# Performance work log

Hardware: AMD Instinct MI355X
Metric: run time of the kernel (lower is better)

## Reference

```python
import jax, jax.numpy as jnp
import numpy as np

B, N, F, H, R = 16, 64, 64, 4, 50
C = F * H  # n_coefficients = n_heads * hidden_features
CUTOFF = 5.0  # ExpNormalSmearing cutoff_upper (cutoff_lower = 0)


def _dense(k, fin, fout):
    s = 1.0 / np.sqrt(fin)
    return jax.random.uniform(k, (fin, fout), jnp.float32, -s, s)


def setup_inputs() -> dict:
    key = jax.random.key(0)
    ks = jax.random.split(key, 20)
    start = float(np.exp(-CUTOFF))
    return {
        "h": jax.random.normal(ks[0], (B, N, F), jnp.float32),
        "x": jax.random.normal(ks[1], (B, N, 3), jnp.float32),
        "v": jax.random.normal(ks[2], (B, N, 3), jnp.float32) * 0.1,
        # edge model (ContinuousFilterConvolutionWithConcatenation)
        "W_in": _dense(ks[3], 2 * F, R), "b_in": jnp.zeros((R,), jnp.float32),
        "rbf_means": jnp.linspace(start, 1.0, R).astype(jnp.float32),
        "rbf_betas": jnp.full((R,), (2.0 / R * (1.0 - start)) ** -2, jnp.float32),
        "W_e1": _dense(ks[4], 2 * F + R + 1, F), "b_e1": jnp.zeros((F,), jnp.float32),
        "W_e2": _dense(ks[5], F, F), "b_e2": jnp.zeros((F,), jnp.float32),
        # semantic attention
        "W_sem": _dense(ks[6], F, H), "b_sem": jnp.zeros((H,), jnp.float32),
        "log_gamma": -jnp.log(jnp.linspace(1.0, 5.0, H)).astype(jnp.float32),
        # spatial attention
        "W_xmix": _dense(ks[7], C, C),
        "W_post1": _dense(ks[8], C, F), "b_post1": jnp.zeros((F,), jnp.float32),
        "W_post2": _dense(ks[9], F, F), "b_post2": jnp.zeros((F,), jnp.float32),
        # node update
        "W_node1": _dense(ks[10], F + C + F, F), "b_node1": jnp.zeros((F,), jnp.float32),
        "W_node2": _dense(ks[11], F, F), "b_node2": jnp.zeros((F,), jnp.float32),
        # velocity update
        "W_vel1": _dense(ks[12], F, F), "b_vel1": jnp.zeros((F,), jnp.float32),
        "W_vel2": _dense(ks[13], F, 1),
        "W_vmix": _dense(ks[14], C, 1),
    }


def reference(h, x, v, W_in, b_in, rbf_means, rbf_betas, W_e1, b_e1, W_e2, b_e2,
              W_sem, b_sem, log_gamma, W_xmix, W_post1, b_post1, W_post2, b_post2,
              W_node1, b_node1, W_node2, b_node2, W_vel1, b_vel1, W_vel2, W_vmix):
    silu = jax.nn.silu
    n = h.shape[-2]
    # pairwise displacement x_j - x_i : (B, N, N, 3)
    x_minus_xt = x[..., None, :, :] - x[..., :, None, :]
    d = jnp.sqrt(jax.nn.relu((x_minus_xt ** 2).sum(-1, keepdims=True)) + 1e-5)  # (B,N,N,1)
    # pairwise node features [h_j, h_i] : (B, N, N, 2F)
    hj = jnp.broadcast_to(h[..., None, :, :], h.shape[:-2] + (n, n, h.shape[-1]))
    hi = jnp.broadcast_to(h[..., :, None, :], hj.shape)
    h_cat = jnp.concatenate([hj, hi], -1)
    # edge model: RBF-smeared continuous-filter conv with concatenation
    h_mid = h_cat @ W_in + b_in  # (B,N,N,R)
    cut = 0.5 * (jnp.cos(d * (jnp.pi / CUTOFF)) + 1.0) * (d < CUTOFF)
    rbf = cut * jnp.exp(-rbf_betas * (jnp.exp(-d) - rbf_means) ** 2)  # (B,N,N,R)
    h_e = jnp.concatenate([h_cat, rbf * h_mid, d], -1)
    h_e = silu(h_e @ W_e1 + b_e1) @ W_e2 + b_e2  # (B,N,N,F)
    # attentions, softmax over neighbor axis (-2), diagonal masked out
    eye = jnp.eye(n, dtype=h.dtype)[:, :, None]
    sem = jax.nn.celu(h_e @ W_sem + b_sem, alpha=2.0) - 1e5 * eye
    sem = jax.nn.softmax(sem, axis=-2)  # (B,N,N,H)
    euc = jax.nn.softmax(-(d + 1e5 * eye) * jnp.exp(log_gamma), axis=-2)  # (B,N,N,H)
    att = euc * sem
    att = att / att.sum(-2, keepdims=True)
    # per-head attention-weighted edge features, flattened (F outer, H inner)
    h_e_att = (h_e[..., :, None] * att[..., None, :]).reshape(att.shape[:-1] + (F * H,))
    # spatial attention on unit displacement vectors
    coeff = jnp.tanh(h_e_att @ W_xmix)  # (B,N,N,C)
    x_hat = x_minus_xt / (d + 1e-5)
    comb = x_hat[..., None, :] * coeff[..., None]  # (B,N,N,C,3)
    comb_sum = comb.mean(axis=-3)  # mean over neighbors -> (B,N,C,3)
    h_comb = (comb_sum ** 2).sum(-1)  # invariant squared norms (B,N,C)
    h_comb = silu(silu(h_comb @ W_post1 + b_post1) @ W_post2 + b_post2)
    # node update (residual)
    h_agg = h_e_att.sum(axis=-2)  # (B,N,C)
    h_out = h + silu(silu(jnp.concatenate([h, h_agg, h_comb], -1) @ W_node1 + b_node1) @ W_node2 + b_node2)
    # equivariant velocity / coordinate update
    delta_v = jnp.einsum('...ijcd,c->...id', comb, W_vmix[:, 0]) / n  # v_mixing + mean over j
    gate = 2.0 * jax.nn.sigmoid(silu(h_out @ W_vel1 + b_vel1) @ W_vel2)  # double_sigmoid, (B,N,1)
    v_out = delta_v + gate * v
    x_out = x + v_out
    return h_out, x_out, v_out
```

## Files before the change

### kernel.cpp

```cpp
#include <hip/hip_runtime.h>
#include <math.h>

#define NB 16
#define NN 64
#define NF 64
#define NH 4
#define NR 50
#define NC 256

typedef __attribute__((ext_vector_type(8))) short short8;
typedef __attribute__((ext_vector_type(4))) float f32x4;

#define WS_WE1R 0
#define WS_WE2  4096
#define WS_WX   8192
#define WS_PO1  73728
#define WS_NO1  90112
#define WS_PO2  114688
#define WS_NO2  118784
#define WS_VE1  122880
#define MID_F   65536
#define E1_F    (MID_F + 131072)
#define HAGG_F  (E1_F + 131072)
#define COMB_F  (HAGG_F + 262144)

__device__ __forceinline__ float siluf(float x) { return x / (1.f + __expf(-x)); }
__device__ __forceinline__ float tanhfast(float x) { return 1.f - 2.f / (__expf(2.f * x) + 1.f); }

__device__ __forceinline__ short f2bfs(float f) {
    __bf16 b = (__bf16)f;
    union { __bf16 b; short s; } u; u.b = b; return u.s;
}
__device__ __forceinline__ float bf1(ushort u) {
    union { unsigned u; float f; } c; c.u = ((unsigned)u) << 16; return c.f;
}
__device__ __forceinline__ float bflo(unsigned u) {
    union { unsigned u; float f; } c; c.u = u << 16; return c.f;
}
__device__ __forceinline__ float bfhi(unsigned u) {
    union { unsigned u; float f; } c; c.u = u & 0xFFFF0000u; return c.f;
}

__device__ __forceinline__ float wave_max(float v) {
#pragma unroll
    for (int s = 32; s >= 1; s >>= 1) v = fmaxf(v, __shfl_xor(v, s));
    return v;
}
__device__ __forceinline__ float wave_sum(float v) {
#pragma unroll
    for (int s = 32; s >= 1; s >>= 1) v += __shfl_xor(v, s);
    return v;
}

__global__ __launch_bounds__(256)
void prep_kernel(const float* __restrict__ W_e1, const float* __restrict__ b_e1,
                 const float* __restrict__ W_e2, const float* __restrict__ W_xmix,
                 const float* __restrict__ W_post1, const float* __restrict__ W_node1,
                 const float* __restrict__ W_post2, const float* __restrict__ W_node2,
                 const float* __restrict__ W_vel1,
                 const float* __restrict__ h, const float* __restrict__ W_in,
                 const float* __restrict__ b_in,
                 short* __restrict__ wpack, float* __restrict__ mid_T, float* __restrict__ e1)
{
    int blk = blockIdx.x, t = threadIdx.x;
    if (blk < 62) {
        int s = blk * 256 + t;
        short8 val;
        if (s < 512) {
            int cl = s & 15, g = (s >> 4) & 3, q = s >> 6;
            int ks = q & 1, nt = q >> 1;
            int c = nt * 16 + cl, k0 = 32 * ks + 8 * g;
#pragma unroll
            for (int i = 0; i < 8; i++) {
                int kr = k0 + i;
                float f = (kr < 50) ? W_e1[(128 + kr) * NF + c] : (kr == 50 ? W_e1[178 * NF + c] : 0.f);
                val[i] = f2bfs(f);
            }
            *(short8*)(&wpack[WS_WE1R + s * 8]) = val;
        } else if (s < 1024) {
            int u = s - 512;
            int cl = u & 15, g = (u >> 4) & 3, q = u >> 6;
            int ks = q & 1, nt = q >> 1;
            int c = nt * 16 + cl, k0 = 32 * ks + 8 * g;
#pragma unroll
            for (int i = 0; i < 8; i++) val[i] = f2bfs(W_e2[(k0 + i) * NF + c]);
            *(short8*)(&wpack[WS_WE2 + u * 8]) = val;
        } else if (s < 9216) {
            int u = s - 1024;
            int cl = u & 15, g = (u >> 4) & 3, q = u >> 6;
            int ks = q & 7, wn = q >> 3;
            int c = (wn >> 2) * 64 + (wn & 3) * 16 + cl, k0 = 32 * ks + 8 * g;
#pragma unroll
            for (int i = 0; i < 8; i++) val[i] = f2bfs(W_xmix[(k0 + i) * NC + c]);
            *(short8*)(&wpack[WS_WX + u * 8]) = val;
        } else if (s < 11264) {
            int u = s - 9216;
            int cl = u & 15, g = (u >> 4) & 3, q = u >> 6;
            int ks = q & 7, nt = q >> 3;
            int c = nt * 16 + cl, k0 = 32 * ks + 8 * g;
#pragma unroll
            for (int i = 0; i < 8; i++) val[i] = f2bfs(W_post1[(k0 + i) * NF + c]);
            *(short8*)(&wpack[WS_PO1 + u * 8]) = val;
        } else if (s < 14336) {
            int u = s - 11264;
            int cl = u & 15, g = (u >> 4) & 3, q = u >> 6;
            int ks = q % 12, nt = q / 12;
            int c = nt * 16 + cl, k0 = 32 * ks + 8 * g;
#pragma unroll
            for (int i = 0; i < 8; i++) val[i] = f2bfs(W_node1[(k0 + i) * NF + c]);
            *(short8*)(&wpack[WS_NO1 + u * 8]) = val;
        } else if (s < 14848) {
            int u = s - 14336;
            int cl = u & 15, g = (u >> 4) & 3, q = u >> 6;
            int ks = q & 1, nt = q >> 1;
            int c = nt * 16 + cl, k0 = 32 * ks + 8 * g;
#pragma unroll
            for (int i = 0; i < 8; i++) val[i] = f2bfs(W_post2[(k0 + i) * NF + c]);
            *(short8*)(&wpack[WS_PO2 + u * 8]) = val;
        } else if (s < 15360) {
            int u = s - 14848;
            int cl = u & 15, g = (u >> 4) & 3, q = u >> 6;
            int ks = q & 1, nt = q >> 1;
            int c = nt * 16 + cl, k0 = 32 * ks + 8 * g;
#pragma unroll
            for (int i = 0; i < 8; i++) val[i] = f2bfs(W_node2[(k0 + i) * NF + c]);
            *(short8*)(&wpack[WS_NO2 + u * 8]) = val;
        } else {
            int u = s - 15360;
            int cl = u & 15, g = (u >> 4) & 3, q = u >> 6;
            int ks = q & 1, nt = q >> 1;
            int c = nt * 16 + cl, k0 = 32 * ks + 8 * g;
#pragma unroll
            for (int i = 0; i < 8; i++) val[i] = f2bfs(W_vel1[(k0 + i) * NF + c]);
            *(short8*)(&wpack[WS_VE1 + u * 8]) = val;
        }
    } else {
        int node = blk - 62;
        __shared__ float s_hn[64];
        if (t < 64) s_hn[t] = h[node * NF + t];
        __syncthreads();
        if (t < 64) {
            float acc = 0.f;
#pragma unroll 8
            for (int k = 0; k < 64; k++) acc += s_hn[k] * W_e1[k * NF + t];
            e1[node * 128 + t] = acc;
        } else if (t < 128) {
            int f = t - 64;
            float acc = b_e1[f];
#pragma unroll 8
            for (int k = 0; k < 64; k++) acc += s_hn[k] * W_e1[(64 + k) * NF + f];
            e1[node * 128 + 64 + f] = acc;
        } else if (t < 178) {
            int r = t - 128;
            float acc = 0.f;
#pragma unroll 8
            for (int k = 0; k < 64; k++) acc += s_hn[k] * W_in[k * NR + r];
            mid_T[r * 1024 + node] = acc;
        } else if (t >= 192 && t < 242) {
            int r = t - 192;
            float acc = b_in[r];
#pragma unroll 8
            for (int k = 0; k < 64; k++) acc += s_hn[k] * W_in[(64 + k) * NR + r];
            mid_T[(64 + r) * 1024 + node] = acc;
        }
    }
}

__global__ __launch_bounds__(256)
void sake_edge_kernel(
    const float* __restrict__ x,
    const float* __restrict__ mid_T, const float* __restrict__ e1,
    const float* __restrict__ rbf_means, const float* __restrict__ rbf_betas,
    const float* __restrict__ b_e2,
    const float* __restrict__ W_sem, const float* __restrict__ b_sem,
    const float* __restrict__ log_gamma,
    const short* __restrict__ wpack,
    float* __restrict__ hagg_g, float* __restrict__ comb_g)
{
    const int bi = blockIdx.x;
    const int b  = bi >> 6;
    const int i  = bi & 63;
    const int t  = threadIdx.x;
    const int w  = t >> 6, l = t & 63, lr = l & 15, lg = l >> 4;

    __shared__ __align__(16) short s_A[16 * 64 * 8];
    __shared__ __align__(16) short s_he[64 * 72];
    __shared__ float s_xhat[256];
    __shared__ float s_att[256];
    __shared__ float s_wsem[256];
    __shared__ float s_midi[52];

    const short8* A8  = (const short8*)s_A;
    short8*       A8w = (short8*)s_A;
    const short8* We1p = (const short8*)(wpack + WS_WE1R);
    const short8* We2p = (const short8*)(wpack + WS_WE2);
    const short8* Wxp  = (const short8*)(wpack + WS_WX);

    s_wsem[t] = W_sem[t];
    if (t < 50) s_midi[t] = mid_T[(64 + t) * 1024 + b * 64 + i];
    if (t < 64) {
        int j = t;
        float dx = x[(b * NN + j) * 3 + 0] - x[(b * NN + i) * 3 + 0];
        float dy = x[(b * NN + j) * 3 + 1] - x[(b * NN + i) * 3 + 1];
        float dz = x[(b * NN + j) * 3 + 2] - x[(b * NN + i) * 3 + 2];
        float d2 = dx * dx + dy * dy + dz * dz;
        float d  = sqrtf(fmaxf(d2, 0.f) + 1e-5f);
        float inv = 1.f / (d + 1e-5f);
        s_xhat[j * 4 + 0] = dx * inv;
        s_xhat[j * 4 + 1] = dy * inv;
        s_xhat[j * 4 + 2] = dz * inv;
        s_xhat[j * 4 + 3] = d;
    }
    __syncthreads();

    {
        int j = t & 63, p = t >> 6;
        float d = s_xhat[j * 4 + 3];
        float cut = 0.5f * (__cosf(d * 0.6283185307179586f) + 1.f) * (d < 5.f ? 1.f : 0.f);
        float emd = __expf(-d);
        const float* mcol = mid_T + b * 64 + j;
#pragma unroll
        for (int q = 0; q < 2; q++) {
            int sl = 2 * p + q;
            short8 val;
#pragma unroll
            for (int e = 0; e < 8; e++) {
                int r = sl * 8 + e;
                float o;
                if (r < 50) {
                    float m = mcol[r * 1024] + s_midi[r];
                    float df = emd - rbf_means[r];
                    o = cut * __expf(-rbf_betas[r] * df * df) * m;
                } else if (r == 50) o = d;
                else o = 0.f;
                val[e] = f2bfs(o);
            }
            A8w[sl * 64 + j] = val;
        }
    }
    __syncthreads();

    {
        int f = w * 16 + lr;
        const float* e1b = e1 + (size_t)b * 64 * 128;
        float e1i_v = e1b[i * 128 + 64 + f];
        f32x4 acc[4];
#pragma unroll
        for (int jt = 0; jt < 4; jt++)
#pragma unroll
            for (int r = 0; r < 4; r++) {
                int j = jt * 16 + lg * 4 + r;
                acc[jt][r] = e1b[j * 128 + f] + e1i_v;
            }
#pragma unroll
        for (int ks = 0; ks < 2; ks++) {
            short8 bb = We1p[(w * 2 + ks) * 64 + l];
#pragma unroll
            for (int jt = 0; jt < 4; jt++) {
                short8 aa = A8[(ks * 4 + lg) * 64 + jt * 16 + lr];
                acc[jt] = __builtin_amdgcn_mfma_f32_16x16x32_bf16(aa, bb, acc[jt], 0, 0, 0);
            }
        }
#pragma unroll
        for (int jt = 0; jt < 4; jt++)
#pragma unroll
            for (int r = 0; r < 4; r++) {
                int j = jt * 16 + lg * 4 + r;
                s_A[(((f >> 3) + 8) * 64 + j) * 8 + (f & 7)] = f2bfs(siluf(acc[jt][r]));
            }
        __syncthreads();
    }

    {
        f32x4 acc[4];
#pragma unroll
        for (int jt = 0; jt < 4; jt++) { acc[jt][0] = 0.f; acc[jt][1] = 0.f; acc[jt][2] = 0.f; acc[jt][3] = 0.f; }
#pragma unroll
        for (int ks = 0; ks < 2; ks++) {
            short8 bb = We2p[(w * 2 + ks) * 64 + l];
#pragma unroll
            for (int jt = 0; jt < 4; jt++) {
                short8 aa = A8[((8 + ks * 4 + lg)) * 64 + jt * 16 + lr];
                acc[jt] = __builtin_amdgcn_mfma_f32_16x16x32_bf16(aa, bb, acc[jt], 0, 0, 0);
            }
        }
        float be2 = b_e2[w * 16 + lr];
        int f = w * 16 + lr;
#pragma unroll
        for (int jt = 0; jt < 4; jt++)
#pragma unroll
            for (int r = 0; r < 4; r++) {
                int j = jt * 16 + lg * 4 + r;
                s_he[j * 72 + f] = f2bfs(acc[jt][r] + be2);
            }
        __syncthreads();
    }

    {
        int hh = w, j = l;
        const short8* hrow = (const short8*)(s_he + j * 72);
        float acc = b_sem[hh];
#pragma unroll
        for (int q = 0; q < 8; q++) {
            short8 hv = hrow[q];
#pragma unroll
            for (int e = 0; e < 8; e++)
                acc += bf1((ushort)hv[e]) * s_wsem[(q * 8 + e) * 4 + hh];
        }
        float cel = fmaxf(acc, 0.f) + fminf(0.f, 2.f * (__expf(0.5f * acc) - 1.f));
        float diag = (j == i) ? 1e5f : 0.f;
        float slog = cel - diag;
        float m1 = wave_max(slog);
        float e1v = __expf(slog - m1);
        float sem = e1v / wave_sum(e1v);
        float gam = __expf(log_gamma[hh]);
        float elog = -(s_xhat[j * 4 + 3] + diag) * gam;
        float m2 = wave_max(elog);
        float e2 = __expf(elog - m2);
        float euc = e2 / wave_sum(e2);
        float a = sem * euc;
        a = a / wave_sum(a);
        s_att[j * 4 + hh] = a;
    }
    __syncthreads();

    {
        int f2 = t >> 3, hh = (t >> 1) & 3, jh = t & 1;
        float a0 = 0.f, a1 = 0.f;
#pragma unroll 8
        for (int jj = 0; jj < 32; jj++) {
            int j = jh * 32 + jj;
            float at = s_att[j * 4 + hh];
            unsigned u = *(const unsigned*)(s_he + j * 72 + 2 * f2);
            a0 += bflo(u) * at;
            a1 += bfhi(u) * at;
        }
        a0 += __shfl_xor(a0, 1);
        a1 += __shfl_xor(a1, 1);
        if (!jh) {
            hagg_g[bi * 256 + (2 * f2) * 4 + hh]     = a0;
            hagg_g[bi * 256 + (2 * f2 + 1) * 4 + hh] = a1;
        }
    }

    f32x4 acc[4][4];
#pragma unroll
    for (int jt = 0; jt < 4; jt++)
#pragma unroll
        for (int nt = 0; nt < 4; nt++) { acc[jt][nt][0] = 0.f; acc[jt][nt][1] = 0.f; acc[jt][nt][2] = 0.f; acc[jt][nt][3] = 0.f; }

    for (int half = 0; half < 2; half++) {
        {
            int j = t & 63, kc = t >> 6;
            float a0 = s_att[j * 4 + 0], a1 = s_att[j * 4 + 1];
            float a2 = s_att[j * 4 + 2], a3 = s_att[j * 4 + 3];
            short8 hv = *(const short8*)(s_he + j * 72 + (half * 32 + kc * 8));
#pragma unroll
            for (int s = 0; s < 4; s++) {
                int sl = kc * 4 + s;
                float h0 = bf1((ushort)hv[2 * s]), h1 = bf1((ushort)hv[2 * s + 1]);
                short8 val;
                val[0] = f2bfs(h0 * a0); val[1] = f2bfs(h0 * a1);
                val[2] = f2bfs(h0 * a2); val[3] = f2bfs(h0 * a3);
                val[4] = f2bfs(h1 * a0); val[5] = f2bfs(h1 * a1);
                val[6] = f2bfs(h1 * a2); val[7] = f2bfs(h1 * a3);
                A8w[sl * 64 + j] = val;
            }
        }
        __syncthreads();
#pragma unroll
        for (int ks = 0; ks < 4; ks++) {
            short8 aa[4], bb[4];
#pragma unroll
            for (int jt = 0; jt < 4; jt++) aa[jt] = A8[(ks * 4 + lg) * 64 + jt * 16 + lr];
#pragma unroll
            for (int nt = 0; nt < 4; nt++) bb[nt] = Wxp[((w * 4 + nt) * 8 + half * 4 + ks) * 64 + l];
#pragma unroll
            for (int jt = 0; jt < 4; jt++)
#pragma unroll
                for (int nt = 0; nt < 4; nt++)
                    acc[jt][nt] = __builtin_amdgcn_mfma_f32_16x16x32_bf16(aa[jt], bb[nt], acc[jt][nt], 0, 0, 0);
        }
        __syncthreads();
    }

    {
#pragma unroll
        for (int nt = 0; nt < 4; nt++) {
            float p0 = 0.f, p1 = 0.f, p2 = 0.f;
#pragma unroll
            for (int jt = 0; jt < 4; jt++)
#pragma unroll
                for (int r = 0; r < 4; r++) {
                    int j = jt * 16 + lg * 4 + r;
                    float th = tanhfast(acc[jt][nt][r]);
                    p0 += s_xhat[j * 4 + 0] * th;
                    p1 += s_xhat[j * 4 + 1] * th;
                    p2 += s_xhat[j * 4 + 2] * th;
                }
            p0 += __shfl_xor(p0, 16); p0 += __shfl_xor(p0, 32);
            p1 += __shfl_xor(p1, 16); p1 += __shfl_xor(p1, 32);
            p2 += __shfl_xor(p2, 16); p2 += __shfl_xor(p2, 32);
            if (lg == 0) {
                int c = w * 64 + nt * 16 + lr;
                float* cg = comb_g + bi * 768 + c * 3;
                cg[0] = p0 * (1.f / 64.f);
                cg[1] = p1 * (1.f / 64.f);
                cg[2] = p2 * (1.f / 64.f);
            }
        }
    }
}

__global__ __launch_bounds__(256)
void sake_tail_kernel(
    const float* __restrict__ h, const float* __restrict__ x, const float* __restrict__ v,
    const float* __restrict__ hagg_g, const float* __restrict__ comb_g,
    const float* __restrict__ b_post1, const float* __restrict__ b_post2,
    const float* __restrict__ b_node1, const float* __restrict__ b_node2,
    const float* __restrict__ b_vel1,
    const float* __restrict__ W_vel2, const float* __restrict__ W_vmix,
    const short* __restrict__ wpack,
    float* __restrict__ out_h, float* __restrict__ out_x, float* __restrict__ out_v)
{
    const int g0 = blockIdx.x * 16;
    const int t = threadIdx.x;
    const int w = t >> 6, l = t & 63, lr = l & 15, lg = l >> 4;

    __shared__ __align__(16) short s_Aa[88 * 16 * 8];
    __shared__ float s_wv[256];
    __shared__ float s_wv2[64];
    __shared__ float s_red[4][16];

    const short8* A8  = (const short8*)s_Aa;
    const short8* PO1p = (const short8*)(wpack + WS_PO1);
    const short8* NO1p = (const short8*)(wpack + WS_NO1);
    const short8* PO2p = (const short8*)(wpack + WS_PO2);
    const short8* NO2p = (const short8*)(wpack + WS_NO2);
    const short8* VE1p = (const short8*)(wpack + WS_VE1);

    {
        s_wv[t] = W_vmix[t];
        if (t < 64) s_wv2[t] = W_vel2[t];
        int n = t & 15, c0 = (t >> 4) * 16;
        const float* cg = comb_g + (g0 + n) * 768;
        const float* ha = hagg_g + (g0 + n) * 256;
#pragma unroll
        for (int cc = 0; cc < 16; cc++) {
            int c = c0 + cc;
            float v0 = cg[c * 3 + 0], v1 = cg[c * 3 + 1], v2 = cg[c * 3 + 2];
            float hcp = v0 * v0 + v1 * v1 + v2 * v2;
            s_Aa[((c >> 3) * 16 + n) * 8 + (c & 7)] = f2bfs(hcp);
            s_Aa[((40 + (c >> 3)) * 16 + n) * 8 + (c & 7)] = f2bfs(ha[c]);
        }
        int f0 = (t >> 4) * 4;
#pragma unroll
        for (int ff = 0; ff < 4; ff++) {
            int f = f0 + ff;
            s_Aa[((32 + (f >> 3)) * 16 + n) * 8 + (f & 7)] = f2bfs(h[(g0 + n) * 64 + f]);
        }
    }
    __syncthreads();

    {
        f32x4 acc = {0.f, 0.f, 0.f, 0.f};
#pragma unroll
        for (int ks = 0; ks < 8; ks++) {
            short8 aa = A8[(ks * 4 + lg) * 16 + lr];
            short8 bb = PO1p[((w * 8 + ks) * 4 + lg) * 16 + lr];
            acc = __builtin_amdgcn_mfma_f32_16x16x32_bf16(aa, bb, acc, 0, 0, 0);
        }
        int f = w * 16 + lr;
        float bp = b_post1[f];
        __syncthreads();
#pragma unroll
        for (int r = 0; r < 4; r++) {
            int n = lg * 4 + r;
            s_Aa[((80 + (f >> 3)) * 16 + n) * 8 + (f & 7)] = f2bfs(siluf(acc[r] + bp));
        }
        __syncthreads();
    }

    {
        f32x4 acc = {0.f, 0.f, 0.f, 0.f};
#pragma unroll
        for (int ks = 0; ks < 2; ks++) {
            short8 aa = A8[((80 + ks * 4 + lg)) * 16 + lr];
            short8 bb = PO2p[((w * 2 + ks) * 4 + lg) * 16 + lr];
            acc = __builtin_amdgcn_mfma_f32_16x16x32_bf16(aa, bb, acc, 0, 0, 0);
        }
        int f = w * 16 + lr;
        float bp = b_post2[f];
#pragma unroll
        for (int r = 0; r < 4; r++) {
            int n = lg * 4 + r;
            s_Aa[((72 + (f >> 3)) * 16 + n) * 8 + (f & 7)] = f2bfs(siluf(acc[r] + bp));
        }
        __syncthreads();
    }

    {
        f32x4 acc = {0.f, 0.f, 0.f, 0.f};
#pragma unroll
        for (int ks = 0; ks < 12; ks++) {
            short8 aa = A8[((32 + ks * 4 + lg)) * 16 + lr];
            short8 bb = NO1p[((w * 12 + ks) * 4 + lg) * 16 + lr];
            acc = __builtin_amdgcn_mfma_f32_16x16x32_bf16(aa, bb, acc, 0, 0, 0);
        }
        int f = w * 16 + lr;
        float bp = b_node1[f];
#pragma unroll
        for (int r = 0; r < 4; r++) {
            int n = lg * 4 + r;
            s_Aa[((f >> 3) * 16 + n) * 8 + (f & 7)] = f2bfs(siluf(acc[r] + bp));
        }
        __syncthreads();
    }

    {
        f32x4 acc = {0.f, 0.f, 0.f, 0.f};
#pragma unroll
        for (int ks = 0; ks < 2; ks++) {
            short8 aa = A8[(ks * 4 + lg) * 16 + lr];
            short8 bb = NO2p[((w * 2 + ks) * 4 + lg) * 16 + lr];
            acc = __builtin_amdgcn_mfma_f32_16x16x32_bf16(aa, bb, acc, 0, 0, 0);
        }
        int f = w * 16 + lr;
        float bp = b_node2[f];
#pragma unroll
        for (int r = 0; r < 4; r++) {
            int n = lg * 4 + r;
            float ho = h[(g0 + n) * 64 + f] + siluf(acc[r] + bp);
            out_h[(g0 + n) * 64 + f] = ho;
            s_Aa[((8 + (f >> 3)) * 16 + n) * 8 + (f & 7)] = f2bfs(ho);
        }
        __syncthreads();
    }

    {
        f32x4 acc = {0.f, 0.f, 0.f, 0.f};
#pragma unroll
        for (int ks = 0; ks < 2; ks++) {
            short8 aa = A8[((8 + ks * 4 + lg)) * 16 + lr];
            short8 bb = VE1p[((w * 2 + ks) * 4 + lg) * 16 + lr];
            acc = __builtin_amdgcn_mfma_f32_16x16x32_bf16(aa, bb, acc, 0, 0, 0);
        }
        int f = w * 16 + lr;
        float bp = b_vel1[f];
        float wv2 = s_wv2[f];
#pragma unroll
        for (int r = 0; r < 4; r++) {
            float p = siluf(acc[r] + bp) * wv2;
            p += __shfl_xor(p, 1); p += __shfl_xor(p, 2);
            p += __shfl_xor(p, 4); p += __shfl_xor(p, 8);
            if (lr == 0) s_red[w][lg * 4 + r] = p;
        }
        __syncthreads();
    }

    {
        int n = t >> 4, q = t & 15;
        float p0 = 0.f, p1 = 0.f, p2 = 0.f;
        const float* cg = comb_g + (g0 + n) * 768;
#pragma unroll
        for (int cc = 0; cc < 16; cc++) {
            int c = q * 16 + cc;
            float wv = s_wv[c];
            p0 += cg[c * 3 + 0] * wv;
            p1 += cg[c * 3 + 1] * wv;
            p2 += cg[c * 3 + 2] * wv;
        }
        p0 += __shfl_xor(p0, 1); p0 += __shfl_xor(p0, 2); p0 += __shfl_xor(p0, 4); p0 += __shfl_xor(p0, 8);
        p1 += __shfl_xor(p1, 1); p1 += __shfl_xor(p1, 2); p1 += __shfl_xor(p1, 4); p1 += __shfl_xor(p1, 8);
        p2 += __shfl_xor(p2, 1); p2 += __shfl_xor(p2, 2); p2 += __shfl_xor(p2, 4); p2 += __shfl_xor(p2, 8);
        if (q == 0) {
            float g = s_red[0][n] + s_red[1][n] + s_red[2][n] + s_red[3][n];
            g = 2.f / (1.f + __expf(-g));
            float dv0 = p0 + g * v[(g0 + n) * 3 + 0];
            float dv1 = p1 + g * v[(g0 + n) * 3 + 1];
            float dv2 = p2 + g * v[(g0 + n) * 3 + 2];
            out_v[(g0 + n) * 3 + 0] = dv0;
            out_v[(g0 + n) * 3 + 1] = dv1;
            out_v[(g0 + n) * 3 + 2] = dv2;
            out_x[(g0 + n) * 3 + 0] = x[(g0 + n) * 3 + 0] + dv0;
            out_x[(g0 + n) * 3 + 1] = x[(g0 + n) * 3 + 1] + dv1;
            out_x[(g0 + n) * 3 + 2] = x[(g0 + n) * 3 + 2] + dv2;
        }
    }
}

extern "C" void kernel_launch(void* const* d_in, const int* in_sizes, int n_in,
                              void* d_out, int out_size, void* d_ws, size_t ws_size,
                              hipStream_t stream) {
    const float* h        = (const float*)d_in[0];
    const float* x        = (const float*)d_in[1];
    const float* v        = (const float*)d_in[2];
    const float* W_in     = (const float*)d_in[3];
    const float* b_in     = (const float*)d_in[4];
    const float* rbf_m    = (const float*)d_in[5];
    const float* rbf_b    = (const float*)d_in[6];
    const float* W_e1     = (const float*)d_in[7];
    const float* b_e1     = (const float*)d_in[8];
    const float* W_e2     = (const float*)d_in[9];
    const float* b_e2     = (const float*)d_in[10];
    const float* W_sem    = (const float*)d_in[11];
    const float* b_sem    = (const float*)d_in[12];
    const float* log_g    = (const float*)d_in[13];
    const float* W_xmix   = (const float*)d_in[14];
    const float* W_post1  = (const float*)d_in[15];
    const float* b_post1  = (const float*)d_in[16];
    const float* W_post2  = (const float*)d_in[17];
    const float* b_post2  = (const float*)d_in[18];
    const float* W_node1  = (const float*)d_in[19];
    const float* b_node1  = (const float*)d_in[20];
    const float* W_node2  = (const float*)d_in[21];
    const float* b_node2  = (const float*)d_in[22];
    const float* W_vel1   = (const float*)d_in[23];
    const float* b_vel1   = (const float*)d_in[24];
    const float* W_vel2   = (const float*)d_in[25];
    const float* W_vmix   = (const float*)d_in[26];

    float* out   = (float*)d_out;
    float* out_h = out;
    float* out_x = out + NB * NN * NF;
    float* out_v = out + NB * NN * NF + NB * NN * 3;

    short* wpack = (short*)d_ws;
    float* wsf   = (float*)d_ws;
    float* mid_T = wsf + MID_F;
    float* e1    = wsf + E1_F;
    float* hagg  = wsf + HAGG_F;
    float* comb  = wsf + COMB_F;

    prep_kernel<<<62 + 1024, 256, 0, stream>>>(
        W_e1, b_e1, W_e2, W_xmix, W_post1, W_node1, W_post2, W_node2, W_vel1,
        h, W_in, b_in, wpack, mid_T, e1);

    sake_edge_kernel<<<NB * NN, 256, 0, stream>>>(
        x, mid_T, e1, rbf_m, rbf_b, b_e2, W_sem, b_sem, log_g,
        wpack, hagg, comb);

    sake_tail_kernel<<<64, 256, 0, stream>>>(
        h, x, v, hagg, comb,
        b_post1, b_post2, b_node1, b_node2, b_vel1,
        W_vel2, W_vmix, wpack, out_h, out_x, out_v);
}
```

Baseline: 58.16 us.

## Factor attention out of xmix GEMM and split into separate parallel kernel

Folds the semantic-attention projection into the W_e2 matmul by precomputing W_e2·W_sem and its bias. Reorders W_xmix so the per-head attention weights are applied after a K=64 GEMM over raw edge features rather than a K=256 GEMM over the head-expanded product, then sums heads via lane shuffles before tanh. Moves this step into a new kernel with four blocks per node, passing h_e, attention and unit vectors through global memory. This cuts matmul FLOPs and raises parallelism, at the cost of an extra launch and a global-memory round trip.

```diff
diff --git a/kernel.cpp b/kernel.cpp
--- a/kernel.cpp
+++ b/kernel.cpp
@@ -13,16 +13,20 @@
 
 #define WS_WE1R 0
 #define WS_WE2  4096
-#define WS_WX   8192
-#define WS_PO1  73728
-#define WS_NO1  90112
-#define WS_PO2  114688
-#define WS_NO2  118784
-#define WS_VE1  122880
-#define MID_F   65536
+#define WS_WX   9216
+#define WS_PO1  74752
+#define WS_NO1  91136
+#define WS_PO2  115712
+#define WS_NO2  119808
+#define WS_VE1  123904
+#define MID_F   64000
 #define E1_F    (MID_F + 131072)
 #define HAGG_F  (E1_F + 131072)
 #define COMB_F  (HAGG_F + 262144)
+#define ATT_F   (COMB_F + 786432)
+#define XHAT_F  (ATT_F + 262144)
+#define BS2_F   (XHAT_F + 262144)
+#define HE_S    ((BS2_F + 8) * 2)
 
 __device__ __forceinline__ float siluf(float x) { return x / (1.f + __expf(-x)); }
 __device__ __forceinline__ float tanhfast(float x) { return 1.f - 2.f / (__expf(2.f * x) + 1.f); }
@@ -54,17 +58,21 @@
 
 __global__ __launch_bounds__(256)
 void prep_kernel(const float* __restrict__ W_e1, const float* __restrict__ b_e1,
-                 const float* __restrict__ W_e2, const float* __restrict__ W_xmix,
+                 const float* __restrict__ W_e2, const float* __restrict__ b_e2,
+                 const float* __restrict__ W_sem, const float* __restrict__ b_sem,
+                 const float* __restrict__ W_xmix,
                  const float* __restrict__ W_post1, const float* __restrict__ W_node1,
                  const float* __restrict__ W_post2, const float* __restrict__ W_node2,
                  const float* __restrict__ W_vel1,
                  const float* __restrict__ h, const float* __restrict__ W_in,
                  const float* __restrict__ b_in,
-                 short* __restrict__ wpack, float* __restrict__ mid_T, float* __restrict__ e1)
+                 short* __restrict__ wpack, float* __restrict__ mid_T,
+                 float* __restrict__ e1, float* __restrict__ bs2)
 {
     int blk = blockIdx.x, t = threadIdx.x;
-    if (blk < 62) {
+    if (blk < 63) {
         int s = blk * 256 + t;
+        if (s >= 16000) return;
         short8 val;
         if (s < 512) {
             int cl = s & 15, g = (s >> 4) & 3, q = s >> 6;
@@ -77,48 +85,65 @@
                 val[i] = f2bfs(f);
             }
             *(short8*)(&wpack[WS_WE1R + s * 8]) = val;
-        } else if (s < 1024) {
+        } else if (s < 1152) {
             int u = s - 512;
             int cl = u & 15, g = (u >> 4) & 3, q = u >> 6;
             int ks = q & 1, nt = q >> 1;
             int c = nt * 16 + cl, k0 = 32 * ks + 8 * g;
 #pragma unroll
-            for (int i = 0; i < 8; i++) val[i] = f2bfs(W_e2[(k0 + i) * NF + c]);
+            for (int i = 0; i < 8; i++) {
+                int k = k0 + i;
+                float f;
+                if (c < 64) f = W_e2[k * NF + c];
+                else {
+                    int cc = c - 64;
+                    if (cc < 4) {
+                        f = 0.f;
+                        for (int m = 0; m < 64; m++) f += W_e2[k * NF + m] * W_sem[m * NH + cc];
+                    } else f = 0.f;
+                }
+                val[i] = f2bfs(f);
+            }
             *(short8*)(&wpack[WS_WE2 + u * 8]) = val;
-        } else if (s < 9216) {
-            int u = s - 1024;
-            int cl = u & 15, g = (u >> 4) & 3, q = u >> 6;
-            int ks = q & 7, wn = q >> 3;
-            int c = (wn >> 2) * 64 + (wn & 3) * 16 + cl, k0 = 32 * ks + 8 * g;
-#pragma unroll
-            for (int i = 0; i < 8; i++) val[i] = f2bfs(W_xmix[(k0 + i) * NC + c]);
+        } else if (s < 9344) {
+            int u = s - 1152;
+            int l = u & 63, ks = (u >> 6) & 1, nt = (u >> 7) & 3, w = (u >> 9) & 3, q = u >> 11;
+            int lr = l & 15;
+            int c = q * 64 + w * 16 + nt * 4 + (lr >> 2);
+            int hh = lr & 3;
+            int k0 = ks * 32 + (l >> 4) * 8;
+#pragma unroll
+            for (int i = 0; i < 8; i++) {
+                int f = k0 + i;
+                val[i] = f2bfs(W_xmix[(f * 4 + hh) * NC + c]);
+            }
             *(short8*)(&wpack[WS_WX + u * 8]) = val;
-        } else if (s < 11264) {
-            int u = s - 9216;
+        } else if (s < 11392) {
+            int u = s - 9344;
             int cl = u & 15, g = (u >> 4) & 3, q = u >> 6;
             int ks = q & 7, nt = q >> 3;
             int c = nt * 16 + cl, k0 = 32 * ks + 8 * g;
 #pragma unroll
             for (int i = 0; i < 8; i++) val[i] = f2bfs(W_post1[(k0 + i) * NF + c]);
             *(short8*)(&wpack[WS_PO1 + u * 8]) = val;
-        } else if (s < 14336) {
-            int u = s - 11264;
+        } else if (s < 14464) {
+            int u = s - 11392;
             int cl = u & 15, g = (u >> 4) & 3, q = u >> 6;
             int ks = q % 12, nt = q / 12;
             int c = nt * 16 + cl, k0 = 32 * ks + 8 * g;
 #pragma unroll
             for (int i = 0; i < 8; i++) val[i] = f2bfs(W_node1[(k0 + i) * NF + c]);
             *(short8*)(&wpack[WS_NO1 + u * 8]) = val;
-        } else if (s < 14848) {
-            int u = s - 14336;
+        } else if (s < 14976) {
+            int u = s - 14464;
             int cl = u & 15, g = (u >> 4) & 3, q = u >> 6;
             int ks = q & 1, nt = q >> 1;
             int c = nt * 16 + cl, k0 = 32 * ks + 8 * g;
 #pragma unroll
             for (int i = 0; i < 8; i++) val[i] = f2bfs(W_post2[(k0 + i) * NF + c]);
             *(short8*)(&wpack[WS_PO2 + u * 8]) = val;
-        } else if (s < 15360) {
-            int u = s - 14848;
+        } else if (s < 15488) {
+            int u = s - 14976;
             int cl = u & 15, g = (u >> 4) & 3, q = u >> 6;
             int ks = q & 1, nt = q >> 1;
             int c = nt * 16 + cl, k0 = 32 * ks + 8 * g;
@@ -126,7 +151,7 @@
             for (int i = 0; i < 8; i++) val[i] = f2bfs(W_node2[(k0 + i) * NF + c]);
             *(short8*)(&wpack[WS_NO2 + u * 8]) = val;
         } else {
-            int u = s - 15360;
+            int u = s - 15488;
             int cl = u & 15, g = (u >> 4) & 3, q = u >> 6;
             int ks = q & 1, nt = q >> 1;
             int c = nt * 16 + cl, k0 = 32 * ks + 8 * g;
@@ -134,8 +159,14 @@
             for (int i = 0; i < 8; i++) val[i] = f2bfs(W_vel1[(k0 + i) * NF + c]);
             *(short8*)(&wpack[WS_VE1 + u * 8]) = val;
         }
+    } else if (blk == 63) {
+        if (t < 4) {
+            float acc = b_sem[t];
+            for (int m = 0; m < 64; m++) acc += b_e2[m] * W_sem[m * NH + t];
+            bs2[t] = acc;
+        }
     } else {
-        int node = blk - 62;
+        int node = blk - 64;
         __shared__ float s_hn[64];
         if (t < 64) s_hn[t] = h[node * NF + t];
         __syncthreads();
@@ -171,11 +202,11 @@
     const float* __restrict__ x,
     const float* __restrict__ mid_T, const float* __restrict__ e1,
     const float* __restrict__ rbf_means, const float* __restrict__ rbf_betas,
-    const float* __restrict__ b_e2,
-    const float* __restrict__ W_sem, const float* __restrict__ b_sem,
+    const float* __restrict__ b_e2, const float* __restrict__ bs2,
     const float* __restrict__ log_gamma,
     const short* __restrict__ wpack,
-    float* __restrict__ hagg_g, float* __restrict__ comb_g)
+    float* __restrict__ hagg_g, float* __restrict__ att_g,
+    float* __restrict__ xhat_g, short* __restrict__ heg)
 {
     const int bi = blockIdx.x;
     const int b  = bi >> 6;
@@ -187,16 +218,14 @@
     __shared__ __align__(16) short s_he[64 * 72];
     __shared__ float s_xhat[256];
     __shared__ float s_att[256];
-    __shared__ float s_wsem[256];
+    __shared__ float s_sem[256];
     __shared__ float s_midi[52];
 
     const short8* A8  = (const short8*)s_A;
     short8*       A8w = (short8*)s_A;
     const short8* We1p = (const short8*)(wpack + WS_WE1R);
     const short8* We2p = (const short8*)(wpack + WS_WE2);
-    const short8* Wxp  = (const short8*)(wpack + WS_WX);
-
-    s_wsem[t] = W_sem[t];
+
     if (t < 50) s_midi[t] = mid_T[(64 + t) * 1024 + b * 64 + i];
     if (t < 64) {
         int j = t;
@@ -214,6 +243,7 @@
     __syncthreads();
 
     {
+        xhat_g[bi * 256 + t] = s_xhat[t];
         int j = t & 63, p = t >> 6;
         float d = s_xhat[j * 4 + 3];
         float cut = 0.5f * (__cosf(d * 0.6283185307179586f) + 1.f) * (d < 5.f ? 1.f : 0.f);
@@ -272,16 +302,22 @@
     }
 
     {
-        f32x4 acc[4];
-#pragma unroll
-        for (int jt = 0; jt < 4; jt++) { acc[jt][0] = 0.f; acc[jt][1] = 0.f; acc[jt][2] = 0.f; acc[jt][3] = 0.f; }
+        f32x4 acc[4], acc2[4];
+#pragma unroll
+        for (int jt = 0; jt < 4; jt++) {
+            acc[jt][0] = 0.f; acc[jt][1] = 0.f; acc[jt][2] = 0.f; acc[jt][3] = 0.f;
+            acc2[jt][0] = 0.f; acc2[jt][1] = 0.f; acc2[jt][2] = 0.f; acc2[jt][3] = 0.f;
+        }
 #pragma unroll
         for (int ks = 0; ks < 2; ks++) {
             short8 bb = We2p[(w * 2 + ks) * 64 + l];
+            short8 bb2 = We2p[(8 + ks) * 64 + l];
 #pragma unroll
             for (int jt = 0; jt < 4; jt++) {
                 short8 aa = A8[((8 + ks * 4 + lg)) * 64 + jt * 16 + lr];
                 acc[jt] = __builtin_amdgcn_mfma_f32_16x16x32_bf16(aa, bb, acc[jt], 0, 0, 0);
+                if (w == 0)
+                    acc2[jt] = __builtin_amdgcn_mfma_f32_16x16x32_bf16(aa, bb2, acc2[jt], 0, 0, 0);
             }
         }
         float be2 = b_e2[w * 16 + lr];
@@ -293,20 +329,32 @@
                 int j = jt * 16 + lg * 4 + r;
                 s_he[j * 72 + f] = f2bfs(acc[jt][r] + be2);
             }
-        __syncthreads();
-    }
-
+        if (w == 0 && lr < 4) {
+#pragma unroll
+            for (int jt = 0; jt < 4; jt++)
+#pragma unroll
+                for (int r = 0; r < 4; r++) {
+                    int j = jt * 16 + lg * 4 + r;
+                    s_sem[j * 4 + lr] = acc2[jt][r];
+                }
+        }
+        __syncthreads();
+    }
+
+    {
+        short8* hegw = (short8*)heg;
+#pragma unroll
+        for (int p = 0; p < 2; p++) {
+            int a = p * 256 + t;
+            int jt = a >> 7, ks = (a >> 6) & 1, li = a & 63;
+            int j = jt * 16 + (li & 15);
+            int k0 = ks * 32 + ((li >> 4) & 3) * 8;
+            hegw[(size_t)bi * 512 + a] = *(const short8*)(s_he + j * 72 + k0);
+        }
+    }
     {
         int hh = w, j = l;
-        const short8* hrow = (const short8*)(s_he + j * 72);
-        float acc = b_sem[hh];
-#pragma unroll
-        for (int q = 0; q < 8; q++) {
-            short8 hv = hrow[q];
-#pragma unroll
-            for (int e = 0; e < 8; e++)
-                acc += bf1((ushort)hv[e]) * s_wsem[(q * 8 + e) * 4 + hh];
-        }
+        float acc = s_sem[j * 4 + hh] + bs2[hh];
         float cel = fmaxf(acc, 0.f) + fminf(0.f, 2.f * (__expf(0.5f * acc) - 1.f));
         float diag = (j == i) ? 1e5f : 0.f;
         float slog = cel - diag;
@@ -325,6 +373,7 @@
     __syncthreads();
 
     {
+        att_g[bi * 256 + t] = s_att[t];
         int f2 = t >> 3, hh = (t >> 1) & 3, jh = t & 1;
         float a0 = 0.f, a1 = 0.f;
 #pragma unroll 8
@@ -342,6 +391,33 @@
             hagg_g[bi * 256 + (2 * f2 + 1) * 4 + hh] = a1;
         }
     }
+}
+
+__global__ __launch_bounds__(256)
+void sake_xmix_kernel(
+    const short* __restrict__ wpack, const float* __restrict__ att_g,
+    const float* __restrict__ xhat_g, const short* __restrict__ heg,
+    float* __restrict__ comb_g)
+{
+    const int blk = blockIdx.x;
+    const int bi = blk >> 2, q = blk & 3;
+    const int t = threadIdx.x;
+    const int w = t >> 6, l = t & 63, lr = l & 15, lg = l >> 4;
+
+    __shared__ __align__(16) short s_A[512 * 8];
+    __shared__ float s_att[256];
+    __shared__ float s_xh[256];
+
+    const short8* A8 = (const short8*)s_A;
+    short8* A8w = (short8*)s_A;
+    const short8* hep = (const short8*)(heg) + (size_t)bi * 512;
+    const short8* Wxp = (const short8*)(wpack + WS_WX);
+
+    A8w[t] = hep[t];
+    A8w[256 + t] = hep[256 + t];
+    s_att[t] = att_g[bi * 256 + t];
+    s_xh[t] = xhat_g[bi * 256 + t];
+    __syncthreads();
 
     f32x4 acc[4][4];
 #pragma unroll
@@ -349,64 +425,50 @@
 #pragma unroll
         for (int nt = 0; nt < 4; nt++) { acc[jt][nt][0] = 0.f; acc[jt][nt][1] = 0.f; acc[jt][nt][2] = 0.f; acc[jt][nt][3] = 0.f; }
 
-    for (int half = 0; half < 2; half++) {
-        {
-            int j = t & 63, kc = t >> 6;
-            float a0 = s_att[j * 4 + 0], a1 = s_att[j * 4 + 1];
-            float a2 = s_att[j * 4 + 2], a3 = s_att[j * 4 + 3];
-            short8 hv = *(const short8*)(s_he + j * 72 + (half * 32 + kc * 8));
-#pragma unroll
-            for (int s = 0; s < 4; s++) {
-                int sl = kc * 4 + s;
-                float h0 = bf1((ushort)hv[2 * s]), h1 = bf1((ushort)hv[2 * s + 1]);
-                short8 val;
-                val[0] = f2bfs(h0 * a0); val[1] = f2bfs(h0 * a1);
-                val[2] = f2bfs(h0 * a2); val[3] = f2bfs(h0 * a3);
-                val[4] = f2bfs(h1 * a0); val[5] = f2bfs(h1 * a1);
-                val[6] = f2bfs(h1 * a2); val[7] = f2bfs(h1 * a3);
-                A8w[sl * 64 + j] = val;
-            }
-        }
-        __syncthreads();
-#pragma unroll
-        for (int ks = 0; ks < 4; ks++) {
-            short8 aa[4], bb[4];
-#pragma unroll
-            for (int jt = 0; jt < 4; jt++) aa[jt] = A8[(ks * 4 + lg) * 64 + jt * 16 + lr];
-#pragma unroll
-            for (int nt = 0; nt < 4; nt++) bb[nt] = Wxp[((w * 4 + nt) * 8 + half * 4 + ks) * 64 + l];
+#pragma unroll
+    for (int ks = 0; ks < 2; ks++) {
+        short8 aa[4];
+#pragma unroll
+        for (int jt = 0; jt < 4; jt++) aa[jt] = A8[(jt * 2 + ks) * 64 + l];
+#pragma unroll
+        for (int nt = 0; nt < 4; nt++) {
+            short8 bb = Wxp[((((q * 4 + w) * 4 + nt) * 2) + ks) * 64 + l];
 #pragma unroll
             for (int jt = 0; jt < 4; jt++)
-#pragma unroll
-                for (int nt = 0; nt < 4; nt++)
-                    acc[jt][nt] = __builtin_amdgcn_mfma_f32_16x16x32_bf16(aa[jt], bb[nt], acc[jt][nt], 0, 0, 0);
-        }
-        __syncthreads();
-    }
-
-    {
-#pragma unroll
-        for (int nt = 0; nt < 4; nt++) {
-            float p0 = 0.f, p1 = 0.f, p2 = 0.f;
-#pragma unroll
-            for (int jt = 0; jt < 4; jt++)
-#pragma unroll
-                for (int r = 0; r < 4; r++) {
-                    int j = jt * 16 + lg * 4 + r;
-                    float th = tanhfast(acc[jt][nt][r]);
-                    p0 += s_xhat[j * 4 + 0] * th;
-                    p1 += s_xhat[j * 4 + 1] * th;
-                    p2 += s_xhat[j * 4 + 2] * th;
-                }
-            p0 += __shfl_xor(p0, 16); p0 += __shfl_xor(p0, 32);
-            p1 += __shfl_xor(p1, 16); p1 += __shfl_xor(p1, 32);
-            p2 += __shfl_xor(p2, 16); p2 += __shfl_xor(p2, 32);
-            if (lg == 0) {
-                int c = w * 64 + nt * 16 + lr;
-                float* cg = comb_g + bi * 768 + c * 3;
-                cg[0] = p0 * (1.f / 64.f);
-                cg[1] = p1 * (1.f / 64.f);
-                cg[2] = p2 * (1.f / 64.f);
+                acc[jt][nt] = __builtin_amdgcn_mfma_f32_16x16x32_bf16(aa[jt], bb, acc[jt][nt], 0, 0, 0);
+        }
+    }
+
+    float p[4][3];
+#pragma unroll
+    for (int nt = 0; nt < 4; nt++) { p[nt][0] = 0.f; p[nt][1] = 0.f; p[nt][2] = 0.f; }
+    int hh = lr & 3;
+#pragma unroll
+    for (int jt = 0; jt < 4; jt++)
+#pragma unroll
+        for (int r = 0; r < 4; r++) {
+            int j = jt * 16 + lg * 4 + r;
+            float ax = s_xh[j * 4 + 0], ay = s_xh[j * 4 + 1], az = s_xh[j * 4 + 2];
+            float at = s_att[j * 4 + hh];
+#pragma unroll
+            for (int nt = 0; nt < 4; nt++) {
+                float s = at * acc[jt][nt][r];
+                s += __shfl_xor(s, 1);
+                s += __shfl_xor(s, 2);
+                float th = tanhfast(s);
+                p[nt][0] += ax * th; p[nt][1] += ay * th; p[nt][2] += az * th;
+            }
+        }
+#pragma unroll
+    for (int nt = 0; nt < 4; nt++) {
+#pragma unroll
+        for (int k3 = 0; k3 < 3; k3++) {
+            float val = p[nt][k3];
+            val += __shfl_xor(val, 16);
+            val += __shfl_xor(val, 32);
+            if (lg == 0 && (l & 3) == 0) {
+                int c = q * 64 + w * 16 + nt * 4 + (lr >> 2);
+                comb_g[bi * 768 + c * 3 + k3] = val * (1.f / 64.f);
             }
         }
     }
@@ -480,7 +542,6 @@
         }
         __syncthreads();
     }
-
     {
         f32x4 acc = {0.f, 0.f, 0.f, 0.f};
 #pragma unroll
@@ -498,7 +559,6 @@
         }
         __syncthreads();
     }
-
     {
         f32x4 acc = {0.f, 0.f, 0.f, 0.f};
 #pragma unroll
@@ -516,7 +576,6 @@
         }
         __syncthreads();
     }
-
     {
         f32x4 acc = {0.f, 0.f, 0.f, 0.f};
 #pragma unroll
@@ -536,7 +595,6 @@
         }
         __syncthreads();
     }
-
     {
         f32x4 acc = {0.f, 0.f, 0.f, 0.f};
 #pragma unroll
@@ -550,21 +608,20 @@
         float wv2 = s_wv2[f];
 #pragma unroll
         for (int r = 0; r < 4; r++) {
-            float p = siluf(acc[r] + bp) * wv2;
-            p += __shfl_xor(p, 1); p += __shfl_xor(p, 2);
-            p += __shfl_xor(p, 4); p += __shfl_xor(p, 8);
-            if (lr == 0) s_red[w][lg * 4 + r] = p;
-        }
-        __syncthreads();
-    }
-
-    {
-        int n = t >> 4, q = t & 15;
+            float pv = siluf(acc[r] + bp) * wv2;
+            pv += __shfl_xor(pv, 1); pv += __shfl_xor(pv, 2);
+            pv += __shfl_xor(pv, 4); pv += __shfl_xor(pv, 8);
+            if (lr == 0) s_red[w][lg * 4 + r] = pv;
+        }
+        __syncthreads();
+    }
+    {
+        int n = t >> 4, qq = t & 15;
         float p0 = 0.f, p1 = 0.f, p2 = 0.f;
         const float* cg = comb_g + (g0 + n) * 768;
 #pragma unroll
         for (int cc = 0; cc < 16; cc++) {
-            int c = q * 16 + cc;
+            int c = qq * 16 + cc;
             float wv = s_wv[c];
             p0 += cg[c * 3 + 0] * wv;
             p1 += cg[c * 3 + 1] * wv;
@@ -573,7 +630,7 @@
         p0 += __shfl_xor(p0, 1); p0 += __shfl_xor(p0, 2); p0 += __shfl_xor(p0, 4); p0 += __shfl_xor(p0, 8);
         p1 += __shfl_xor(p1, 1); p1 += __shfl_xor(p1, 2); p1 += __shfl_xor(p1, 4); p1 += __shfl_xor(p1, 8);
         p2 += __shfl_xor(p2, 1); p2 += __shfl_xor(p2, 2); p2 += __shfl_xor(p2, 4); p2 += __shfl_xor(p2, 8);
-        if (q == 0) {
+        if (qq == 0) {
             float g = s_red[0][n] + s_red[1][n] + s_red[2][n] + s_red[3][n];
             g = 2.f / (1.f + __expf(-g));
             float dv0 = p0 + g * v[(g0 + n) * 3 + 0];
@@ -631,14 +688,22 @@
     float* e1    = wsf + E1_F;
     float* hagg  = wsf + HAGG_F;
     float* comb  = wsf + COMB_F;
-
-    prep_kernel<<<62 + 1024, 256, 0, stream>>>(
-        W_e1, b_e1, W_e2, W_xmix, W_post1, W_node1, W_post2, W_node2, W_vel1,
-        h, W_in, b_in, wpack, mid_T, e1);
+    float* att   = wsf + ATT_F;
+    float* xhat  = wsf + XHAT_F;
+    float* bs2   = wsf + BS2_F;
+    short* heg   = wpack + HE_S;
+
+    prep_kernel<<<64 + 1024, 256, 0, stream>>>(
+        W_e1, b_e1, W_e2, b_e2, W_sem, b_sem, W_xmix,
+        W_post1, W_node1, W_post2, W_node2, W_vel1,
+        h, W_in, b_in, wpack, mid_T, e1, bs2);
 
     sake_edge_kernel<<<NB * NN, 256, 0, stream>>>(
-        x, mid_T, e1, rbf_m, rbf_b, b_e2, W_sem, b_sem, log_g,
-        wpack, hagg, comb);
+        x, mid_T, e1, rbf_m, rbf_b, b_e2, bs2, log_g,
+        wpack, hagg, att, xhat, heg);
+
+    sake_xmix_kernel<<<NB * NN * 4, 256, 0, stream>>>(
+        wpack, att, xhat, heg, comb);
 
     sake_tail_kernel<<<64, 256, 0, stream>>>(
         h, x, v, hagg, comb,
```

Result: slower. 117.3 us (+101.8%).

## Batch node projections in prep kernel and re-pad edge-kernel shared buffers

Applied to the files above, without the earlier changes.

The prep kernel now computes four nodes per block, one per wave, and stores the W_in projections row-major per node instead of transposed, so it launches far fewer blocks. The edge kernel reads that new layout. It pads the h_e shared tile from a row stride of 72 to 66 bf16 to avoid bank conflicts on column reads. It writes the first MLP's activations back over the RBF input slots, which needs an extra barrier, and the hagg reduction becomes one thread per output element. The per-j reads of mid are now strided by 128 floats where they were contiguous before, and the prep kernel relies on wave-level visibility of shared memory without a barrier.

```diff
diff --git a/kernel.cpp b/kernel.cpp
--- a/kernel.cpp
+++ b/kernel.cpp
@@ -60,7 +60,7 @@
                  const float* __restrict__ W_vel1,
                  const float* __restrict__ h, const float* __restrict__ W_in,
                  const float* __restrict__ b_in,
-                 short* __restrict__ wpack, float* __restrict__ mid_T, float* __restrict__ e1)
+                 short* __restrict__ wpack, float* __restrict__ mid, float* __restrict__ e1)
 {
     int blk = blockIdx.x, t = threadIdx.x;
     if (blk < 62) {
@@ -135,33 +135,29 @@
             *(short8*)(&wpack[WS_VE1 + u * 8]) = val;
         }
     } else {
-        int node = blk - 62;
-        __shared__ float s_hn[64];
-        if (t < 64) s_hn[t] = h[node * NF + t];
-        __syncthreads();
-        if (t < 64) {
-            float acc = 0.f;
+        int w = t >> 6, l = t & 63;
+        int node = (blk - 62) * 4 + w;
+        __shared__ float s_hn[4][64];
+        s_hn[w][l] = h[node * NF + l];
+        float a0 = 0.f, a1 = b_e1[l];
 #pragma unroll 8
-            for (int k = 0; k < 64; k++) acc += s_hn[k] * W_e1[k * NF + t];
-            e1[node * 128 + t] = acc;
-        } else if (t < 128) {
-            int f = t - 64;
-            float acc = b_e1[f];
+        for (int k = 0; k < 64; k++) {
+            float hv = s_hn[w][k];
+            a0 += hv * W_e1[k * NF + l];
+            a1 += hv * W_e1[(64 + k) * NF + l];
+        }
+        e1[node * 128 + l] = a0;
+        e1[node * 128 + 64 + l] = a1;
+        if (l < 50) {
+            float m0 = 0.f, m1 = b_in[l];
 #pragma unroll 8
-            for (int k = 0; k < 64; k++) acc += s_hn[k] * W_e1[(64 + k) * NF + f];
-            e1[node * 128 + 64 + f] = acc;
-        } else if (t < 178) {
-            int r = t - 128;
-            float acc = 0.f;
-#pragma unroll 8
-            for (int k = 0; k < 64; k++) acc += s_hn[k] * W_in[k * NR + r];
-            mid_T[r * 1024 + node] = acc;
-        } else if (t >= 192 && t < 242) {
-            int r = t - 192;
-            float acc = b_in[r];
-#pragma unroll 8
-            for (int k = 0; k < 64; k++) acc += s_hn[k] * W_in[(64 + k) * NR + r];
-            mid_T[(64 + r) * 1024 + node] = acc;
+            for (int k = 0; k < 64; k++) {
+                float hv = s_hn[w][k];
+                m0 += hv * W_in[k * NR + l];
+                m1 += hv * W_in[(64 + k) * NR + l];
+            }
+            mid[node * 128 + l] = m0;
+            mid[node * 128 + 64 + l] = m1;
         }
     }
 }
@@ -169,9 +165,9 @@
 __global__ __launch_bounds__(256)
 void sake_edge_kernel(
     const float* __restrict__ x,
-    const float* __restrict__ mid_T, const float* __restrict__ e1,
+    const float* __restrict__ mid, const float* __restrict__ e1,
     const float* __restrict__ rbf_means, const float* __restrict__ rbf_betas,
-    const float* __restrict__ b_e2,
+    const float* __restrict__ b_e1, const float* __restrict__ b_e2,
     const float* __restrict__ W_sem, const float* __restrict__ b_sem,
     const float* __restrict__ log_gamma,
     const short* __restrict__ wpack,
@@ -184,7 +180,8 @@
     const int w  = t >> 6, l = t & 63, lr = l & 15, lg = l >> 4;
 
     __shared__ __align__(16) short s_A[16 * 64 * 8];
-    __shared__ __align__(16) short s_he[64 * 72];
+    __shared__ short s_he[64 * 66];
+    __shared__ float s_comb[768];
     __shared__ float s_xhat[256];
     __shared__ float s_att[256];
     __shared__ float s_wsem[256];
@@ -197,7 +194,7 @@
     const short8* Wxp  = (const short8*)(wpack + WS_WX);
 
     s_wsem[t] = W_sem[t];
-    if (t < 50) s_midi[t] = mid_T[(64 + t) * 1024 + b * 64 + i];
+    if (t < 50) s_midi[t] = mid[(b * 64 + i) * 128 + 64 + t];
     if (t < 64) {
         int j = t;
         float dx = x[(b * NN + j) * 3 + 0] - x[(b * NN + i) * 3 + 0];
@@ -218,7 +215,7 @@
         float d = s_xhat[j * 4 + 3];
         float cut = 0.5f * (__cosf(d * 0.6283185307179586f) + 1.f) * (d < 5.f ? 1.f : 0.f);
         float emd = __expf(-d);
-        const float* mcol = mid_T + b * 64 + j;
+        const float* midj = mid + (b * 64 + j) * 128;
 #pragma unroll
         for (int q = 0; q < 2; q++) {
             int sl = 2 * p + q;
@@ -228,7 +225,7 @@
                 int r = sl * 8 + e;
                 float o;
                 if (r < 50) {
-                    float m = mcol[r * 1024] + s_midi[r];
+                    float m = midj[r] + s_midi[r];
                     float df = emd - rbf_means[r];
                     o = cut * __expf(-rbf_betas[r] * df * df) * m;
                 } else if (r == 50) o = d;
@@ -261,12 +258,13 @@
                 acc[jt] = __builtin_amdgcn_mfma_f32_16x16x32_bf16(aa, bb, acc[jt], 0, 0, 0);
             }
         }
+        __syncthreads();
 #pragma unroll
         for (int jt = 0; jt < 4; jt++)
 #pragma unroll
             for (int r = 0; r < 4; r++) {
                 int j = jt * 16 + lg * 4 + r;
-                s_A[(((f >> 3) + 8) * 64 + j) * 8 + (f & 7)] = f2bfs(siluf(acc[jt][r]));
+                s_A[((f >> 3) * 64 + j) * 8 + (f & 7)] = f2bfs(siluf(acc[jt][r]));
             }
         __syncthreads();
     }
@@ -280,7 +278,7 @@
             short8 bb = We2p[(w * 2 + ks) * 64 + l];
 #pragma unroll
             for (int jt = 0; jt < 4; jt++) {
-                short8 aa = A8[((8 + ks * 4 + lg)) * 64 + jt * 16 + lr];
+                short8 aa = A8[(ks * 4 + lg) * 64 + jt * 16 + lr];
                 acc[jt] = __builtin_amdgcn_mfma_f32_16x16x32_bf16(aa, bb, acc[jt], 0, 0, 0);
             }
         }
@@ -291,21 +289,19 @@
 #pragma unroll
             for (int r = 0; r < 4; r++) {
                 int j = jt * 16 + lg * 4 + r;
-                s_he[j * 72 + f] = f2bfs(acc[jt][r] + be2);
+                s_he[j * 66 + f] = f2bfs(acc[jt][r] + be2);
             }
         __syncthreads();
     }
 
     {
         int hh = w, j = l;
-        const short8* hrow = (const short8*)(s_he + j * 72);
         float acc = b_sem[hh];
-#pragma unroll
-        for (int q = 0; q < 8; q++) {
-            short8 hv = hrow[q];
-#pragma unroll
-            for (int e = 0; e < 8; e++)
-                acc += bf1((ushort)hv[e]) * s_wsem[(q * 8 + e) * 4 + hh];
+        const unsigned* hp = (const unsigned*)(s_he + j * 66);
+#pragma unroll 8
+        for (int q = 0; q < 32; q++) {
+            unsigned u = hp[q];
+            acc += bflo(u) * s_wsem[(2 * q) * 4 + hh] + bfhi(u) * s_wsem[(2 * q + 1) * 4 + hh];
         }
         float cel = fmaxf(acc, 0.f) + fminf(0.f, 2.f * (__expf(0.5f * acc) - 1.f));
         float diag = (j == i) ? 1e5f : 0.f;
@@ -325,22 +321,11 @@
     __syncthreads();
 
     {
-        int f2 = t >> 3, hh = (t >> 1) & 3, jh = t & 1;
-        float a0 = 0.f, a1 = 0.f;
+        int f = t >> 2, hh = t & 3;
+        float acc = 0.f;
 #pragma unroll 8
-        for (int jj = 0; jj < 32; jj++) {
-            int j = jh * 32 + jj;
-            float at = s_att[j * 4 + hh];
-            unsigned u = *(const unsigned*)(s_he + j * 72 + 2 * f2);
-            a0 += bflo(u) * at;
-            a1 += bfhi(u) * at;
-        }
-        a0 += __shfl_xor(a0, 1);
-        a1 += __shfl_xor(a1, 1);
-        if (!jh) {
-            hagg_g[bi * 256 + (2 * f2) * 4 + hh]     = a0;
-            hagg_g[bi * 256 + (2 * f2 + 1) * 4 + hh] = a1;
-        }
+        for (int j = 0; j < 64; j++) acc += bf1((ushort)s_he[j * 66 + f]) * s_att[j * 4 + hh];
+        hagg_g[bi * 256 + t] = acc;
     }
 
     f32x4 acc[4][4];
@@ -354,11 +339,12 @@
             int j = t & 63, kc = t >> 6;
             float a0 = s_att[j * 4 + 0], a1 = s_att[j * 4 + 1];
             float a2 = s_att[j * 4 + 2], a3 = s_att[j * 4 + 3];
-            short8 hv = *(const short8*)(s_he + j * 72 + (half * 32 + kc * 8));
 #pragma unroll
             for (int s = 0; s < 4; s++) {
                 int sl = kc * 4 + s;
-                float h0 = bf1((ushort)hv[2 * s]), h1 = bf1((ushort)hv[2 * s + 1]);
+                int kbase = half * 128 + sl * 8;
+                unsigned u = *(const unsigned*)(s_he + j * 66 + (kbase >> 2));
+                float h0 = bflo(u), h1 = bfhi(u);
                 short8 val;
                 val[0] = f2bfs(h0 * a0); val[1] = f2bfs(h0 * a1);
                 val[2] = f2bfs(h0 * a2); val[3] = f2bfs(h0 * a3);
@@ -627,17 +613,17 @@
 
     short* wpack = (short*)d_ws;
     float* wsf   = (float*)d_ws;
-    float* mid_T = wsf + MID_F;
+    float* mid   = wsf + MID_F;
     float* e1    = wsf + E1_F;
     float* hagg  = wsf + HAGG_F;
     float* comb  = wsf + COMB_F;
 
-    prep_kernel<<<62 + 1024, 256, 0, stream>>>(
+    prep_kernel<<<62 + 256, 256, 0, stream>>>(
         W_e1, b_e1, W_e2, W_xmix, W_post1, W_node1, W_post2, W_node2, W_vel1,
-        h, W_in, b_in, wpack, mid_T, e1);
+        h, W_in, b_in, wpack, mid, e1);
 
     sake_edge_kernel<<<NB * NN, 256, 0, stream>>>(
-        x, mid_T, e1, rbf_m, rbf_b, b_e2, W_sem, b_sem, log_g,
+        x, mid, e1, rbf_m, rbf_b, b_e1, b_e2, W_sem, b_sem, log_g,
         wpack, hagg, comb);
 
     sake_tail_kernel<<<64, 256, 0, stream>>>(
```

New measurement: 56.10 us. 1.04x faster.
